# Kernel tuning notes

Measured on AMD Instinct MI355X. Metric: run time of the kernel, lower is better.

## Reference

```python
import jax, jax.numpy as jnp
import numpy as np

B, S, D = 2, 2048, 4096
H, HD = 32, 128  # n_heads, head_dim
P = 30           # prefix_len
ROPE_THETA = 10000.0


def _rope_tables():
    inv = 1.0 / (ROPE_THETA ** (np.arange(0, HD, 2, dtype=np.float64) / HD))
    f = np.outer(np.arange(S, dtype=np.float64), inv)  # [S, HD/2]
    return jnp.asarray(np.cos(f), jnp.float32), jnp.asarray(np.sin(f), jnp.float32)


def setup_inputs() -> dict:
    key = jax.random.key(0)
    ks = jax.random.split(key, 7)
    scale = 0.02
    x = jax.random.normal(ks[0], (B, S, D), jnp.float32)
    freqs_cos, freqs_sin = _rope_tables()
    prefix = jax.random.normal(ks[1], (1, P, D), jnp.float32) * scale
    prefix_gate = jax.random.normal(ks[2], (H,), jnp.float32) * 0.1
    wq = jax.random.normal(ks[3], (D, H * HD), jnp.float32) * scale
    wk = jax.random.normal(ks[4], (D, H * HD), jnp.float32) * scale
    wv = jax.random.normal(ks[5], (D, H * HD), jnp.float32) * scale
    wo = jax.random.normal(ks[6], (H * HD, D), jnp.float32) * scale
    return dict(x=x, freqs_cos=freqs_cos, freqs_sin=freqs_sin, prefix=prefix,
                prefix_gate=prefix_gate, wq=wq, wk=wk, wv=wv, wo=wo, start_pos=0)


def _apply_rope(t, cos, sin):
    # t: [b, s, h, hd]; cos/sin: [s, hd/2] -> broadcast [1, s, 1, hd/2]
    tr = t.reshape(*t.shape[:-1], HD // 2, 2)
    t0, t1 = tr[..., 0], tr[..., 1]
    c = cos[None, :, None, :]
    s = sin[None, :, None, :]
    o0 = t0 * c - t1 * s
    o1 = t0 * s + t1 * c
    return jnp.stack([o0, o1], axis=-1).reshape(t.shape)


def _attend(q, k, v, causal):
    # q: [b, sq, h, d]; k, v: [b, sk, h, d]
    scale = 1.0 / jnp.sqrt(jnp.asarray(HD, q.dtype))
    scores = jnp.einsum('bqhd,bkhd->bhqk', q, k) * scale
    if causal:
        sq, sk = q.shape[1], k.shape[1]
        mask = jnp.tril(jnp.ones((sq, sk), bool))
        scores = jnp.where(mask[None, None], scores, jnp.asarray(-1e30, scores.dtype))
    probs = jax.nn.softmax(scores, axis=-1)
    return jnp.einsum('bhqk,bkhd->bqhd', probs, v)


def reference(x, freqs_cos, freqs_sin, prefix, prefix_gate, wq, wk, wv, wo, start_pos):
    bsz, seqlen, _ = x.shape
    xq = (x @ wq).reshape(bsz, seqlen, H, HD)
    xk = (x @ wk).reshape(bsz, seqlen, H, HD)
    xv = (x @ wv).reshape(bsz, seqlen, H, HD)
    xq = _apply_rope(xq, freqs_cos, freqs_sin)
    xk = _apply_rope(xk, freqs_cos, freqs_sin)
    # n_rep == 1 (MHA), repeat_kv is identity
    out = _attend(xq, xk, xv, causal=True)  # [b, s, h, hd]
    # prefix-tuning branch: no RoPE on prefix k/v, non-causal attention
    pk = jnp.broadcast_to(prefix @ wk, (bsz, P, H * HD)).reshape(bsz, P, H, HD)
    pv = jnp.broadcast_to(prefix @ wv, (bsz, P, H * HD)).reshape(bsz, P, H, HD)
    prefix_delta = _attend(xq, pk, pv, causal=False)
    gate = jnp.tanh(prefix_gate).reshape(1, 1, H, 1)
    out = out + gate * prefix_delta
    out = out.reshape(bsz, seqlen, H * HD)
    return out @ wo
```

## Files before the change

kernel.cpp:

```cpp
#include <hip/hip_runtime.h>
#include <hip/hip_bf16.h>

#define AS1 __attribute__((address_space(1)))
#define AS3 __attribute__((address_space(3)))

typedef __attribute__((ext_vector_type(8))) short bf16x8;
typedef __attribute__((ext_vector_type(4))) float f32x4;

#define B_ 2
#define S_ 2048
#define D_ 4096
#define H_ 32
#define HD_ 128
#define P_ 30

__device__ __forceinline__ short f2b(float f) {
  union { __hip_bfloat16 h; short s; } u;
  u.h = __float2bfloat16(f);
  return u.s;
}
__device__ __forceinline__ float b2f(short s) {
  union { short s; __hip_bfloat16 h; } u;
  u.s = s;
  return __bfloat162float(u.h);
}
__device__ __forceinline__ void gload16(const void* g, void* l) {
  __builtin_amdgcn_global_load_lds((const AS1 void*)g, (AS3 void*)l, 16, 0, 0);
}

__global__ __launch_bounds__(256) void convert_f32_bf16(const float* __restrict__ in,
                                                        short* __restrict__ out) {
  size_t i = ((size_t)blockIdx.x * 256 + threadIdx.x) * 4;
  float4 v = *reinterpret_cast<const float4*>(in + i);
  short4 o;
  o.x = f2b(v.x); o.y = f2b(v.y); o.z = f2b(v.z); o.w = f2b(v.w);
  *reinterpret_cast<short4*>(out + i) = o;
}

__global__ __launch_bounds__(256) void pad_prefix(const float* __restrict__ p,
                                                  short* __restrict__ pb) {
  int i = blockIdx.x * 256 + threadIdx.x;
  int row = i >> 12, col = i & 4095;
  pb[i] = (row < P_) ? f2b(p[row * D_ + col]) : (short)0;
}

__global__ void transpose_convert(const float* __restrict__ W, short* __restrict__ Wt,
                                  int K, int N) {
  __shared__ float t[32][33];
  int bx = blockIdx.x, by = blockIdx.y;
  int tx = threadIdx.x, ty = threadIdx.y;
#pragma unroll
  for (int i = 0; i < 4; ++i) {
    int r = ty * 4 + i;
    t[r][tx] = W[(size_t)(by * 32 + r) * N + bx * 32 + tx];
  }
  __syncthreads();
#pragma unroll
  for (int i = 0; i < 4; ++i) {
    int r = ty * 4 + i;
    Wt[(size_t)(bx * 32 + r) * K + by * 32 + tx] = f2b(t[tx][r]);
  }
}

__global__ __launch_bounds__(256) void rope_kernel(short* __restrict__ q,
                                                   short* __restrict__ k,
                                                   const float* __restrict__ fc,
                                                   const float* __restrict__ fs) {
  short* t = blockIdx.y ? k : q;
  size_t g = ((size_t)blockIdx.x * 256 + threadIdx.x) * 8;
  int d = (int)(g & 127);
  int s = (int)((g >> 12) & 2047);
  bf16x8 v = *reinterpret_cast<bf16x8*>(t + g);
  int i0 = d >> 1;
  float4 c = *reinterpret_cast<const float4*>(fc + (size_t)s * 64 + i0);
  float4 sn = *reinterpret_cast<const float4*>(fs + (size_t)s * 64 + i0);
  float cc[4] = {c.x, c.y, c.z, c.w};
  float ss[4] = {sn.x, sn.y, sn.z, sn.w};
  bf16x8 o;
#pragma unroll
  for (int p = 0; p < 4; ++p) {
    float t0 = b2f(v[2 * p]), t1 = b2f(v[2 * p + 1]);
    o[2 * p] = f2b(t0 * cc[p] - t1 * ss[p]);
    o[2 * p + 1] = f2b(t0 * ss[p] + t1 * cc[p]);
  }
  *reinterpret_cast<bf16x8*>(t + g) = o;
}

template <int OM>
__global__ __launch_bounds__(256) void gemm_bt(const short* __restrict__ A,
                                               const short* __restrict__ Bt,
                                               void* __restrict__ Cv,
                                               int M, int N, int K) {
  __shared__ short As[128 * 32];
  __shared__ short Bs[128 * 32];
  const int tid = threadIdx.x;
  const int lane = tid & 63;
  const int wbase = tid & 192;
  const int wr = ((tid >> 7) & 1) * 64;
  const int wc = ((tid >> 6) & 1) * 64;
  const int lr = lane & 15;
  const int lk = (lane >> 4) * 8;
  int lin = blockIdx.y * gridDim.x + blockIdx.x;
  int nwg = gridDim.x * gridDim.y;
  int cpx = nwg >> 3;
  int swz = (lin & 7) * cpx + (lin >> 3);
  const int bm = swz / gridDim.x, bn = swz % gridDim.x;
  f32x4 acc[4][4] = {};
  const short* Ab = A + (size_t)bm * 128 * K;
  const short* Bb = Bt + (size_t)bn * 128 * K;
  for (int kt = 0; kt < K; kt += 32) {
    __syncthreads();
#pragma unroll
    for (int i = 0; i < 2; ++i) {
      int f = i * 256 + tid;
      int row = f >> 2, col = (f & 3) * 8;
      gload16(Ab + (size_t)row * K + kt + col, &As[(i * 256 + wbase) * 8]);
      gload16(Bb + (size_t)row * K + kt + col, &Bs[(i * 256 + wbase) * 8]);
    }
    __syncthreads();
    bf16x8 af[4], bfr[4];
#pragma unroll
    for (int m = 0; m < 4; ++m)
      af[m] = *reinterpret_cast<const bf16x8*>(&As[(wr + m * 16 + lr) * 32 + lk]);
#pragma unroll
    for (int n = 0; n < 4; ++n)
      bfr[n] = *reinterpret_cast<const bf16x8*>(&Bs[(wc + n * 16 + lr) * 32 + lk]);
#pragma unroll
    for (int m = 0; m < 4; ++m)
#pragma unroll
      for (int n = 0; n < 4; ++n)
        acc[m][n] = __builtin_amdgcn_mfma_f32_16x16x32_bf16(af[m], bfr[n], acc[m][n], 0, 0, 0);
  }
  const int row0 = bm * 128 + wr + (lane >> 4) * 4;
  const int col0 = bn * 128 + wc + lr;
  if constexpr (OM == 3) {
    short* C = (short*)Cv;
#pragma unroll
    for (int m = 0; m < 4; ++m)
#pragma unroll
      for (int n = 0; n < 4; ++n) {
        short4 pk;
        pk.x = f2b(acc[m][n][0]); pk.y = f2b(acc[m][n][1]);
        pk.z = f2b(acc[m][n][2]); pk.w = f2b(acc[m][n][3]);
        size_t idx = (size_t)(col0 + n * 16) * M + row0 + m * 16;
        *reinterpret_cast<short4*>(&C[idx]) = pk;
      }
  } else {
#pragma unroll
    for (int m = 0; m < 4; ++m)
#pragma unroll
      for (int n = 0; n < 4; ++n)
#pragma unroll
        for (int j = 0; j < 4; ++j) {
          size_t idx = (size_t)(row0 + m * 16 + j) * N + col0 + n * 16;
          ((short*)Cv)[idx] = f2b(acc[m][n][j]);
        }
  }
}

#define MFMA16(mh)                                                              \
  _Pragma("unroll") for (int mm = 0; mm < 4; ++mm)                              \
    _Pragma("unroll") for (int nn = 0; nn < 4; ++nn)                            \
      acc[(mh)*4 + mm][nn] = __builtin_amdgcn_mfma_f32_16x16x32_bf16(           \
          af[mm], bf[nn], acc[(mh)*4 + mm][nn], 0, 0, 0);

#define PH_SYNC_PRE                                                             \
  __builtin_amdgcn_s_barrier();                                                 \
  asm volatile("s_waitcnt lgkmcnt(0)" ::: "memory");                            \
  __builtin_amdgcn_sched_barrier(0);                                            \
  __builtin_amdgcn_s_setprio(1);

#define PH_SYNC_POST                                                            \
  __builtin_amdgcn_s_setprio(0);                                                \
  __builtin_amdgcn_s_barrier();

template <int OM>
__global__ __launch_bounds__(512, 2) void gemm256(const short* __restrict__ A,
                                                  const short* __restrict__ Bt,
                                                  void* __restrict__ Cv,
                                                  int M, int N, int K) {
  __shared__ short As[2][256 * 64];
  __shared__ short Bs[2][256 * 64];
  const int tid = threadIdx.x;
  const int w = tid >> 6;
  const int lane = tid & 63;
  const int lr = lane & 15, lg = lane >> 4;
  const int wr = (w >> 2) * 128;
  const int wc = (w & 3) * 64;
  int lin = blockIdx.y * gridDim.x + blockIdx.x;
  int nwg = gridDim.x * gridDim.y;
  int cpx = nwg >> 3;
  int swz = (lin & 7) * cpx + (lin >> 3);
  const int bm = swz / gridDim.x, bn = swz % gridDim.x;

  const short* Ab = A + (size_t)bm * 256 * K;
  const short* Bb = Bt + (size_t)bn * 256 * K;
  const int NT = K >> 6;

  f32x4 acc[8][4] = {};

  auto stA = [&](int slot_, int r0, int kt) {
    int row = r0 + (lane >> 3);
    int gsrc = (lane & 7) ^ ((lane >> 3) & 7);
    gload16(Ab + (size_t)row * K + kt + gsrc * 8, &As[slot_][r0 * 64]);
  };
  auto stB = [&](int slot_, int r0, int kt) {
    int row = r0 + (lane >> 3);
    int gsrc = (lane & 7) ^ ((lane >> 3) & 7);
    gload16(Bb + (size_t)row * K + kt + gsrc * 8, &Bs[slot_][r0 * 64]);
  };

  const int q2 = w * 2, q4 = w * 4;
  const int rt0 = (q2 < 8 ? 0 : 64) + q2 * 8;
  const int rt1 = (q2 + 1 < 8 ? 0 : 64) + (q2 + 1) * 8;

  {
#pragma unroll
    for (int i = 0; i < 4; ++i) stB(0, (q4 + i) * 8, 0);
    stA(0, rt0, 0); stA(0, 64 + rt0, 0);
    stA(0, rt1, 0); stA(0, 64 + rt1, 0);
#pragma unroll
    for (int i = 0; i < 4; ++i) stB(1, (q4 + i) * 8, 64);
    stA(1, rt0, 64); stA(1, 64 + rt0, 64);
    stA(1, rt1, 64); stA(1, 64 + rt1, 64);
  }
  asm volatile("s_waitcnt vmcnt(8)" ::: "memory");
  __builtin_amdgcn_s_barrier();

  for (int t = 0; t < NT; ++t) {
    const int slot = t & 1;
    const int ns = slot ^ 1;
    const int kt1 = (t + 1) << 6, kt2 = (t + 2) << 6;
    const bool s6 = (t >= 1) && (t + 1 < NT);
    const bool s2 = (t + 2 < NT);
    bf16x8 bf[4], af[4];

    {
      const int pg = (lg ^ (lr & 7)) * 8;
#pragma unroll
      for (int nn = 0; nn < 4; ++nn)
        bf[nn] = *(const bf16x8*)&Bs[slot][(wc + nn * 16 + lr) * 64 + pg];
#pragma unroll
      for (int mm = 0; mm < 4; ++mm)
        af[mm] = *(const bf16x8*)&As[slot][(wr + mm * 16 + lr) * 64 + pg];
      if (s6) { stB(ns, (q4 + 0) * 8, kt1); stB(ns, (q4 + 1) * 8, kt1); }
      PH_SYNC_PRE
      MFMA16(0)
      PH_SYNC_POST
    }
    {
      const int pg = (lg ^ (lr & 7)) * 8;
#pragma unroll
      for (int mm = 0; mm < 4; ++mm)
        af[mm] = *(const bf16x8*)&As[slot][(wr + 64 + mm * 16 + lr) * 64 + pg];
      if (s6) { stB(ns, (q4 + 2) * 8, kt1); stB(ns, (q4 + 3) * 8, kt1); }
      PH_SYNC_PRE
      MFMA16(1)
      PH_SYNC_POST
    }
    {
      const int pg = ((4 + lg) ^ (lr & 7)) * 8;
#pragma unroll
      for (int nn = 0; nn < 4; ++nn)
        bf[nn] = *(const bf16x8*)&Bs[slot][(wc + nn * 16 + lr) * 64 + pg];
#pragma unroll
      for (int mm = 0; mm < 4; ++mm)
        af[mm] = *(const bf16x8*)&As[slot][(wr + mm * 16 + lr) * 64 + pg];
      if (s6) { stA(ns, 64 + rt0, kt1); stA(ns, 64 + rt1, kt1); }
      PH_SYNC_PRE
      MFMA16(0)
      PH_SYNC_POST
    }
    {
      const int pg = ((4 + lg) ^ (lr & 7)) * 8;
#pragma unroll
      for (int mm = 0; mm < 4; ++mm)
        af[mm] = *(const bf16x8*)&As[slot][(wr + 64 + mm * 16 + lr) * 64 + pg];
      if (s2) { stA(slot, rt0, kt2); stA(slot, rt1, kt2); }
      PH_SYNC_PRE
      MFMA16(1)
      __builtin_amdgcn_s_setprio(0);
      if (s2) asm volatile("s_waitcnt vmcnt(2)" ::: "memory");
      else    asm volatile("s_waitcnt vmcnt(0)" ::: "memory");
      __builtin_amdgcn_s_barrier();
    }
  }

  const int row0 = bm * 256 + wr + lg * 4;
  const int col0 = bn * 256 + wc + lr;
  if constexpr (OM == 2) {
    short* C = (short*)Cv;
#pragma unroll
    for (int mf = 0; mf < 8; ++mf)
#pragma unroll
      for (int n = 0; n < 4; ++n) {
        int r0 = row0 + mf * 16;
        int bb = r0 >> 11, s0 = r0 & 2047;
        short4 pk;
        pk.x = f2b(acc[mf][n][0]); pk.y = f2b(acc[mf][n][1]);
        pk.z = f2b(acc[mf][n][2]); pk.w = f2b(acc[mf][n][3]);
        size_t idx = ((size_t)(bb * 4096 + col0 + n * 16)) * 2048 + s0;
        *reinterpret_cast<short4*>(&C[idx]) = pk;
      }
  } else {
#pragma unroll
    for (int mf = 0; mf < 8; ++mf)
#pragma unroll
      for (int n = 0; n < 4; ++n)
#pragma unroll
        for (int j = 0; j < 4; ++j) {
          size_t idx = (size_t)(row0 + mf * 16 + j) * N + col0 + n * 16;
          if constexpr (OM == 1) ((short*)Cv)[idx] = f2b(acc[mf][n][j]);
          else ((float*)Cv)[idx] = acc[mf][n][j];
        }
  }
}

__global__ __launch_bounds__(1024, 4) void attn_kernel(
    const short* __restrict__ qb, const short* __restrict__ kb, const short* __restrict__ vt,
    const short* __restrict__ pkb, const short* __restrict__ pvt,
    const float* __restrict__ gate, short* __restrict__ ab) {
  __shared__ short Ks[2][64 * 128];
  __shared__ short Vs[128 * 64];
  __shared__ short Ps[16][16 * 64];
  const int tid = threadIdx.x;
  const int wave = tid >> 6, lane = tid & 63;
  const int lr = lane & 15, lg = lane >> 4;
  const int lin = blockIdx.x;
  const int qt = 7 - (lin >> 6);
  const int bh = lin & 63;
  const int b = bh >> 5, h = bh & 31;

  bf16x8 aq[4];
  {
    const short* qrow = qb + ((size_t)(b * S_ + qt * 256 + wave * 16 + lr) * H_ + h) * HD_;
#pragma unroll
    for (int kk = 0; kk < 4; ++kk)
      aq[kk] = *reinterpret_cast<const bf16x8*>(qrow + kk * 32 + lg * 8);
  }

  float m = -1e30f, l = 0.f, l2 = 0.f;
  f32x4 o[8] = {}, o2[8] = {};

  const short* kb_bh = kb + ((size_t)b * S_ * H_ + h) * HD_;
  const short* vt_bh = vt + ((size_t)(b * H_ + h)) * HD_ * S_;

  auto stageK = [&](int t, int buf) {
    int row = tid >> 4;
    int col = ((tid & 15) ^ (row & 7)) * 8;
    gload16(kb_bh + (size_t)(t * 64 + row) * (H_ * HD_) + col,
            &Ks[buf][(tid & 960) * 8]);
  };
  auto stagePK = [&](int buf) {
    int row = tid >> 4;
    int col = ((tid & 15) ^ (row & 7)) * 8;
    gload16(pkb + (size_t)row * 4096 + h * HD_ + col, &Ks[buf][(tid & 960) * 8]);
  };
  auto loadV = [&](int t, bf16x8& vr) {
    int row = tid >> 3;
    vr = *reinterpret_cast<const bf16x8*>(vt_bh + (size_t)row * S_ + t * 64 + (tid & 7) * 8);
  };
  auto loadPV = [&](bf16x8& vr) {
    int row = tid >> 3;
    vr = *reinterpret_cast<const bf16x8*>(pvt + ((size_t)h * HD_ + row) * 128 + (tid & 7) * 8);
  };
  auto writeV = [&](const bf16x8& vr) {
    int row = tid >> 3;
    int gran = (tid & 7) ^ (row & 7);
    *reinterpret_cast<bf16x8*>(&Vs[row * 64 + gran * 8]) = vr;
  };

  const float scale = 0.08838834764831845f;

  auto qkt = [&](int buf, f32x4 sc[4]) {
    __builtin_amdgcn_s_setprio(1);
#pragma unroll
    for (int cb = 0; cb < 4; ++cb) {
      int tok = cb * 16 + lr;
#pragma unroll
      for (int kk = 0; kk < 4; ++kk) {
        int addr = tok * 128 + (((kk * 4 + lg) ^ (tok & 7)) * 8);
        bf16x8 bk = *reinterpret_cast<const bf16x8*>(&Ks[buf][addr]);
        sc[cb] = __builtin_amdgcn_mfma_f32_16x16x32_bf16(bk, aq[kk], sc[cb], 0, 0, 0);
      }
    }
    __builtin_amdgcn_s_setprio(0);
  };
  auto pv = [&](f32x4* acc_) {
#pragma unroll
    for (int kk = 0; kk < 2; ++kk) {
      bf16x8 ap = *reinterpret_cast<const bf16x8*>(
          &Ps[wave][lr * 64 + (((kk * 4 + lg) ^ (lr & 7)) * 8)]);
      __builtin_amdgcn_s_setprio(1);
#pragma unroll
      for (int nb = 0; nb < 8; ++nb) {
        int d = nb * 16 + lr;
        bf16x8 bv = *reinterpret_cast<const bf16x8*>(
            &Vs[d * 64 + (((kk * 4 + lg) ^ (lr & 7)) * 8)]);
        acc_[nb] = __builtin_amdgcn_mfma_f32_16x16x32_bf16(ap, bv, acc_[nb], 0, 0, 0);
      }
      __builtin_amdgcn_s_setprio(0);
    }
  };

  auto process = [&](int t, bool diag) {
    const int buf = t & 1;
    f32x4 sc[4] = {};
    qkt(buf, sc);
    const int rowg = qt * 256 + wave * 16 + lr;
#pragma unroll
    for (int cb = 0; cb < 4; ++cb)
#pragma unroll
      for (int j = 0; j < 4; ++j) {
        int colg = t * 64 + cb * 16 + lg * 4 + j;
        float v = sc[cb][j] * scale;
        sc[cb][j] = (!diag || colg <= rowg) ? v : -1e30f;
      }
    float mx = sc[0][0];
#pragma unroll
    for (int cb = 0; cb < 4; ++cb)
#pragma unroll
      for (int j = 0; j < 4; ++j) mx = fmaxf(mx, sc[cb][j]);
    mx = fmaxf(mx, __shfl_xor(mx, 16));
    mx = fmaxf(mx, __shfl_xor(mx, 32));
    if (!__all(mx <= m + 8.f)) {
      float mn = fmaxf(m, mx);
      float alpha = __expf(m - mn);
      m = mn;
      l *= alpha;
      f32x4 av;
#pragma unroll
      for (int j = 0; j < 4; ++j) av[j] = __shfl(alpha, lg * 4 + j);
#pragma unroll
      for (int nb = 0; nb < 8; ++nb)
#pragma unroll
        for (int j = 0; j < 4; ++j) o[nb][j] *= av[j];
    }
    float rs = 0.f;
#pragma unroll
    for (int cb = 0; cb < 4; ++cb) {
      short4 pk;
      float p0 = __expf(sc[cb][0] - m);
      float p1 = __expf(sc[cb][1] - m);
      float p2 = __expf(sc[cb][2] - m);
      float p3 = __expf(sc[cb][3] - m);
      rs += (p0 + p1) + (p2 + p3);
      pk.x = f2b(p0); pk.y = f2b(p1); pk.z = f2b(p2); pk.w = f2b(p3);
      int gran = (cb * 2 + (lg >> 1)) ^ (lr & 7);
      *reinterpret_cast<short4*>(&Ps[wave][lr * 64 + gran * 8 + (lg & 1) * 4]) = pk;
    }
    rs += __shfl_xor(rs, 16);
    rs += __shfl_xor(rs, 32);
    l += rs;
    pv(o);
  };

  auto processPrefix = [&]() {
    f32x4 sc[4] = {};
    qkt(0, sc);
#pragma unroll
    for (int cb = 0; cb < 4; ++cb)
#pragma unroll
      for (int j = 0; j < 4; ++j) {
        int coll = cb * 16 + lg * 4 + j;
        float v = sc[cb][j] * scale;
        sc[cb][j] = (coll < P_) ? v : -1e30f;
      }
    float mx = sc[0][0];
#pragma unroll
    for (int cb = 0; cb < 4; ++cb)
#pragma unroll
      for (int j = 0; j < 4; ++j) mx = fmaxf(mx, sc[cb][j]);
    mx = fmaxf(mx, __shfl_xor(mx, 16));
    mx = fmaxf(mx, __shfl_xor(mx, 32));
    float rs = 0.f;
#pragma unroll
    for (int cb = 0; cb < 4; ++cb) {
      short4 pk;
      float p0 = __expf(sc[cb][0] - mx);
      float p1 = __expf(sc[cb][1] - mx);
      float p2 = __expf(sc[cb][2] - mx);
      float p3 = __expf(sc[cb][3] - mx);
      rs += (p0 + p1) + (p2 + p3);
      pk.x = f2b(p0); pk.y = f2b(p1); pk.z = f2b(p2); pk.w = f2b(p3);
      int gran = (cb * 2 + (lg >> 1)) ^ (lr & 7);
      *reinterpret_cast<short4*>(&Ps[wave][lr * 64 + gran * 8 + (lg & 1) * 4]) = pk;
    }
    rs += __shfl_xor(rs, 16);
    rs += __shfl_xor(rs, 32);
    l2 = rs;
    pv(o2);
  };

  const int nt = 4 * (qt + 1);
  bf16x8 vr;

  stagePK(0);
  loadPV(vr);
  __syncthreads();
  writeV(vr);
  __syncthreads();
  processPrefix();
  __syncthreads();

  stageK(0, 0);
  loadV(0, vr);
  __syncthreads();
  writeV(vr);
  __syncthreads();
  for (int t = 0; t < nt; ++t) {
    const bool more = (t + 1 < nt);
    if (more) {
      loadV(t + 1, vr);
      stageK(t + 1, (t + 1) & 1);
    }
    process(t, t >= 4 * qt);
    __syncthreads();
    if (more) writeV(vr);
    __syncthreads();
  }

  {
    float g = tanhf(gate[h]);
    f32x4 lv, lv2;
#pragma unroll
    for (int j = 0; j < 4; ++j) {
      lv[j] = __shfl(l, lg * 4 + j);
      lv2[j] = __shfl(l2, lg * 4 + j);
    }
#pragma unroll
    for (int j = 0; j < 4; ++j) {
      int q = qt * 256 + wave * 16 + lg * 4 + j;
      float inv = 1.f / lv[j];
      float inv2 = g / lv2[j];
      size_t base = ((size_t)(b * S_ + q) * H_ + h) * HD_;
#pragma unroll
      for (int nb = 0; nb < 8; ++nb)
        ab[base + nb * 16 + lr] = f2b(o[nb][j] * inv + o2[nb][j] * inv2);
    }
  }
}

extern "C" void kernel_launch(void* const* d_in, const int* in_sizes, int n_in,
                              void* d_out, int out_size, void* d_ws, size_t ws_size,
                              hipStream_t stream) {
  const float* x = (const float*)d_in[0];
  const float* fc = (const float*)d_in[1];
  const float* fs = (const float*)d_in[2];
  const float* prefix = (const float*)d_in[3];
  const float* gate = (const float*)d_in[4];
  const float* wq = (const float*)d_in[5];
  const float* wk = (const float*)d_in[6];
  const float* wv = (const float*)d_in[7];
  const float* wo = (const float*)d_in[8];
  float* out = (float*)d_out;

  char* ws = (char*)d_ws;
  const size_t SZ = (size_t)4096 * 4096 * 2;
  short* xb = (short*)(ws);
  short* wT = (short*)(ws + SZ);
  short* qbuf = (short*)(ws + 2 * SZ);
  short* kbuf = (short*)(ws + 3 * SZ);
  short* vT = (short*)(ws + 4 * SZ);
  short* pb = (short*)(ws + 5 * SZ);
  short* pkb = (short*)(ws + 5 * SZ + (1 << 20));
  short* pvt = (short*)(ws + 5 * SZ + (2 << 20));
  short* abuf = xb;

  dim3 tcg(128, 128), tcb(32, 8);
  dim3 gg(16, 16), gp(32, 1);

  convert_f32_bf16<<<16384, 256, 0, stream>>>(x, xb);
  pad_prefix<<<2048, 256, 0, stream>>>(prefix, pb);

  transpose_convert<<<tcg, tcb, 0, stream>>>(wq, wT, 4096, 4096);
  gemm256<1><<<gg, 512, 0, stream>>>(xb, wT, qbuf, 4096, 4096, 4096);

  transpose_convert<<<tcg, tcb, 0, stream>>>(wk, wT, 4096, 4096);
  gemm256<1><<<gg, 512, 0, stream>>>(xb, wT, kbuf, 4096, 4096, 4096);
  gemm_bt<1><<<gp, 256, 0, stream>>>(pb, wT, pkb, 128, 4096, 4096);

  transpose_convert<<<tcg, tcb, 0, stream>>>(wv, wT, 4096, 4096);
  gemm256<2><<<gg, 512, 0, stream>>>(xb, wT, vT, 4096, 4096, 4096);
  gemm_bt<3><<<gp, 256, 0, stream>>>(pb, wT, pvt, 128, 4096, 4096);

  rope_kernel<<<dim3(8192, 2), 256, 0, stream>>>(qbuf, kbuf, fc, fs);

  attn_kernel<<<512, 1024, 0, stream>>>(qbuf, kbuf, vT, pkb, pvt, gate, abuf);

  transpose_convert<<<tcg, tcb, 0, stream>>>(wo, wT, 4096, 4096);
  gemm256<0><<<gg, 512, 0, stream>>>(abuf, wT, out, 4096, 4096, 4096);
}
```

Before: 885.6 us.

## Double-buffer V via direct global-to-LDS loads and fold softmax scale into RoPE

The attention kernel now double-buffers V in shared memory and stages it with direct global-to-LDS loads, like K. This removes the register round-trip and one barrier per KV tile, at the cost of an extra 16 KB of LDS per block. The 1/sqrt(d) softmax scale is folded into the RoPE kernel's Q output, so the per-tile scale multiply and non-diagonal mask select go away. The GEMM also issues its A-half prefetch earlier, in the first phase, which changes overlap and VMEM counter timing.

```diff
diff --git a/kernel.cpp b/kernel.cpp
--- a/kernel.cpp
+++ b/kernel.cpp
@@ -67,6 +67,7 @@
                                                    const float* __restrict__ fc,
                                                    const float* __restrict__ fs) {
   short* t = blockIdx.y ? k : q;
+  const float qs = blockIdx.y ? 1.0f : 0.08838834764831845f;
   size_t g = ((size_t)blockIdx.x * 256 + threadIdx.x) * 8;
   int d = (int)(g & 127);
   int s = (int)((g >> 12) & 2047);
@@ -80,8 +81,8 @@
 #pragma unroll
   for (int p = 0; p < 4; ++p) {
     float t0 = b2f(v[2 * p]), t1 = b2f(v[2 * p + 1]);
-    o[2 * p] = f2b(t0 * cc[p] - t1 * ss[p]);
-    o[2 * p + 1] = f2b(t0 * ss[p] + t1 * cc[p]);
+    o[2 * p] = f2b((t0 * cc[p] - t1 * ss[p]) * qs);
+    o[2 * p + 1] = f2b((t0 * ss[p] + t1 * cc[p]) * qs);
   }
   *reinterpret_cast<bf16x8*>(t + g) = o;
 }
@@ -243,7 +244,8 @@
 #pragma unroll
       for (int mm = 0; mm < 4; ++mm)
         af[mm] = *(const bf16x8*)&As[slot][(wr + mm * 16 + lr) * 64 + pg];
-      if (s6) { stB(ns, (q4 + 0) * 8, kt1); stB(ns, (q4 + 1) * 8, kt1); }
+      if (s6) { stB(ns, (q4 + 0) * 8, kt1); stB(ns, (q4 + 1) * 8, kt1);
+                stA(ns, 64 + rt0, kt1);     stA(ns, 64 + rt1, kt1); }
       PH_SYNC_PRE
       MFMA16(0)
       PH_SYNC_POST
@@ -266,7 +268,6 @@
 #pragma unroll
       for (int mm = 0; mm < 4; ++mm)
         af[mm] = *(const bf16x8*)&As[slot][(wr + mm * 16 + lr) * 64 + pg];
-      if (s6) { stA(ns, 64 + rt0, kt1); stA(ns, 64 + rt1, kt1); }
       PH_SYNC_PRE
       MFMA16(0)
       PH_SYNC_POST
@@ -321,7 +322,7 @@
     const short* __restrict__ pkb, const short* __restrict__ pvt,
     const float* __restrict__ gate, short* __restrict__ ab) {
   __shared__ short Ks[2][64 * 128];
-  __shared__ short Vs[128 * 64];
+  __shared__ short Vs[2][128 * 64];
   __shared__ short Ps[16][16 * 64];
   const int tid = threadIdx.x;
   const int wave = tid >> 6, lane = tid & 63;
@@ -356,21 +357,16 @@
     int col = ((tid & 15) ^ (row & 7)) * 8;
     gload16(pkb + (size_t)row * 4096 + h * HD_ + col, &Ks[buf][(tid & 960) * 8]);
   };
-  auto loadV = [&](int t, bf16x8& vr) {
+  auto stageV = [&](int t, int buf) {
     int row = tid >> 3;
-    vr = *reinterpret_cast<const bf16x8*>(vt_bh + (size_t)row * S_ + t * 64 + (tid & 7) * 8);
-  };
-  auto loadPV = [&](bf16x8& vr) {
+    int col = ((tid & 7) ^ (row & 7)) * 8;
+    gload16(vt_bh + (size_t)row * S_ + t * 64 + col, &Vs[buf][(tid & 1016) * 8]);
+  };
+  auto stagePV = [&](int buf) {
     int row = tid >> 3;
-    vr = *reinterpret_cast<const bf16x8*>(pvt + ((size_t)h * HD_ + row) * 128 + (tid & 7) * 8);
-  };
-  auto writeV = [&](const bf16x8& vr) {
-    int row = tid >> 3;
-    int gran = (tid & 7) ^ (row & 7);
-    *reinterpret_cast<bf16x8*>(&Vs[row * 64 + gran * 8]) = vr;
-  };
-
-  const float scale = 0.08838834764831845f;
+    int col = ((tid & 7) ^ (row & 7)) * 8;
+    gload16(pvt + ((size_t)h * HD_ + row) * 128 + col, &Vs[buf][(tid & 1016) * 8]);
+  };
 
   auto qkt = [&](int buf, f32x4 sc[4]) {
     __builtin_amdgcn_s_setprio(1);
@@ -386,7 +382,7 @@
     }
     __builtin_amdgcn_s_setprio(0);
   };
-  auto pv = [&](f32x4* acc_) {
+  auto pv = [&](int buf, f32x4* acc_) {
 #pragma unroll
     for (int kk = 0; kk < 2; ++kk) {
       bf16x8 ap = *reinterpret_cast<const bf16x8*>(
@@ -396,7 +392,7 @@
       for (int nb = 0; nb < 8; ++nb) {
         int d = nb * 16 + lr;
         bf16x8 bv = *reinterpret_cast<const bf16x8*>(
-            &Vs[d * 64 + (((kk * 4 + lg) ^ (lr & 7)) * 8)]);
+            &Vs[buf][d * 64 + (((kk * 4 + lg) ^ (lr & 7)) * 8)]);
         acc_[nb] = __builtin_amdgcn_mfma_f32_16x16x32_bf16(ap, bv, acc_[nb], 0, 0, 0);
       }
       __builtin_amdgcn_s_setprio(0);
@@ -407,15 +403,16 @@
     const int buf = t & 1;
     f32x4 sc[4] = {};
     qkt(buf, sc);
-    const int rowg = qt * 256 + wave * 16 + lr;
-#pragma unroll
-    for (int cb = 0; cb < 4; ++cb)
-#pragma unroll
-      for (int j = 0; j < 4; ++j) {
-        int colg = t * 64 + cb * 16 + lg * 4 + j;
-        float v = sc[cb][j] * scale;
-        sc[cb][j] = (!diag || colg <= rowg) ? v : -1e30f;
-      }
+    if (diag) {
+      const int rowg = qt * 256 + wave * 16 + lr;
+#pragma unroll
+      for (int cb = 0; cb < 4; ++cb)
+#pragma unroll
+        for (int j = 0; j < 4; ++j) {
+          int colg = t * 64 + cb * 16 + lg * 4 + j;
+          if (colg > rowg) sc[cb][j] = -1e30f;
+        }
+    }
     float mx = sc[0][0];
 #pragma unroll
     for (int cb = 0; cb < 4; ++cb)
@@ -452,7 +449,7 @@
     rs += __shfl_xor(rs, 16);
     rs += __shfl_xor(rs, 32);
     l += rs;
-    pv(o);
+    pv(buf, o);
   };
 
   auto processPrefix = [&]() {
@@ -463,8 +460,7 @@
 #pragma unroll
       for (int j = 0; j < 4; ++j) {
         int coll = cb * 16 + lg * 4 + j;
-        float v = sc[cb][j] * scale;
-        sc[cb][j] = (coll < P_) ? v : -1e30f;
+        if (coll >= P_) sc[cb][j] = -1e30f;
       }
     float mx = sc[0][0];
 #pragma unroll
@@ -489,34 +485,26 @@
     rs += __shfl_xor(rs, 16);
     rs += __shfl_xor(rs, 32);
     l2 = rs;
-    pv(o2);
+    pv(0, o2);
   };
 
   const int nt = 4 * (qt + 1);
-  bf16x8 vr;
 
   stagePK(0);
-  loadPV(vr);
-  __syncthreads();
-  writeV(vr);
+  stagePV(0);
   __syncthreads();
   processPrefix();
   __syncthreads();
 
   stageK(0, 0);
-  loadV(0, vr);
-  __syncthreads();
-  writeV(vr);
+  stageV(0, 0);
   __syncthreads();
   for (int t = 0; t < nt; ++t) {
-    const bool more = (t + 1 < nt);
-    if (more) {
-      loadV(t + 1, vr);
+    if (t + 1 < nt) {
       stageK(t + 1, (t + 1) & 1);
+      stageV(t + 1, (t + 1) & 1);
     }
     process(t, t >= 4 * qt);
-    __syncthreads();
-    if (more) writeV(vr);
     __syncthreads();
   }
 
```

Result: no change. 877.3 us (-0.9%).
